# Kernel optimization log

Hardware: AMD Instinct MI355X
Metric: run time of the kernel (lower is better)

Reference implementation:

```python
import jax, jax.numpy as jnp
import numpy as np

EPS = 1e-5
NEG = -1000000000.0

def _layernorm(x, g, b):
    m = x.mean(-1, keepdims=True)
    v = ((x - m) ** 2).mean(-1, keepdims=True)
    return (x - m) / jnp.sqrt(v + EPS) * g + b

D_MODEL, N_HEADS, D_K, D_V, D_FF = 768, 12, 64, 64, 3072
VOCAB, MAX_POS, N_LAYERS = 32000, 2048, 2
B, S = 2, 2048

def setup_inputs() -> dict:
    key = jax.random.key(0)
    ks = jax.random.split(key, 16)
    sc = 0.02
    L = N_LAYERS
    return {
        "inputs": jax.random.randint(ks[0], (B, S), 0, VOCAB, dtype=jnp.int64) if jax.config.jax_enable_x64 else jax.random.randint(ks[0], (B, S), 0, VOCAB, dtype=jnp.int32),
        "attention_mask": jax.random.randint(ks[1], (B, S), 0, 2, dtype=jnp.int32),
        "emb": jax.random.normal(ks[2], (VOCAB, D_MODEL), jnp.float32) * sc,
        "pos_emb": jax.random.normal(ks[3], (MAX_POS, D_MODEL), jnp.float32) * sc,
        "wq": jax.random.normal(ks[4], (L, D_MODEL, N_HEADS * D_K), jnp.float32) * sc,
        "wk": jax.random.normal(ks[5], (L, D_MODEL, N_HEADS * D_K), jnp.float32) * sc,
        "wv": jax.random.normal(ks[6], (L, D_MODEL, N_HEADS * D_V), jnp.float32) * sc,
        "wo": jax.random.normal(ks[7], (L, N_HEADS * D_V, D_MODEL), jnp.float32) * sc,
        "ln1_g": jnp.ones((L, D_MODEL), jnp.float32),
        "ln1_b": jnp.zeros((L, D_MODEL), jnp.float32),
        "w1": jax.random.normal(ks[8], (L, D_MODEL, D_FF), jnp.float32) * sc,
        "b1": jnp.zeros((L, D_FF), jnp.float32),
        "w2": jax.random.normal(ks[9], (L, D_FF, D_MODEL), jnp.float32) * sc,
        "b2": jnp.zeros((L, D_MODEL), jnp.float32),
        "ln2_g": jnp.ones((L, D_MODEL), jnp.float32),
        "ln2_b": jnp.zeros((L, D_MODEL), jnp.float32),
    }

def reference(inputs, attention_mask, emb, pos_emb, wq, wk, wv, wo,
              ln1_g, ln1_b, w1, b1, w2, b2, ln2_g, ln2_b):
    b, s = inputs.shape
    x = emb[inputs] + pos_emb[jnp.arange(s)][None, :, :]  # [B,S,D]
    # combined mask: True where pad token OR strictly-upper (future) position
    sub = jnp.triu(jnp.ones((s, s), dtype=bool), k=1)            # [S,S]
    pad = (attention_mask == 0)[:, None, :]                      # [B,1,S]
    mask = (pad | sub[None, :, :])[:, None, :, :]                # [B,1,S,S] -> broadcast over heads
    # FAITHFUL to source: masked_fill(attention_mask == 0, -1e9) fills where mask is FALSE
    scale = 1.0 / float(np.sqrt(D_K))
    attns = []
    for l in range(N_LAYERS):
        q = (x @ wq[l]).reshape(b, s, N_HEADS, D_K).transpose(0, 2, 1, 3)  # [B,H,S,dk]
        k = (x @ wk[l]).reshape(b, s, N_HEADS, D_K).transpose(0, 2, 1, 3)
        v = (x @ wv[l]).reshape(b, s, N_HEADS, D_V).transpose(0, 2, 1, 3)
        scores = jnp.einsum('bhqd,bhkd->bhqk', q, k) * scale
        scores = jnp.where(mask, scores, NEG)  # fill -1e9 where mask == False (as in source)
        attn = jax.nn.softmax(scores, axis=-1)
        ctx = jnp.einsum('bhqk,bhkd->bhqd', attn, v)
        ctx = ctx.transpose(0, 2, 1, 3).reshape(b, s, N_HEADS * D_V)
        x = _layernorm(ctx @ wo[l] + x, ln1_g[l], ln1_b[l])
        ff = jnp.maximum(x @ w1[l] + b1[l], 0.0) @ w2[l] + b2[l]
        x = _layernorm(ff + x, ln2_g[l], ln2_b[l])
        attns.append(attn)
    return x, jnp.stack(attns)  # [B,S,D], [L,B,H,S,S]
```

## Files before the change

kernel.cpp:

```cpp
#include <hip/hip_runtime.h>
#include <math.h>

#define DM 768
#define NH 12
#define DK 64
#define DFF 3072
#define BB 2
#define SS 2048
#define NL 2

typedef __attribute__((ext_vector_type(8))) short short8;
typedef __attribute__((ext_vector_type(4))) float f32x4;

__device__ inline unsigned short f2bf(float f) {
    unsigned int u = __float_as_uint(f);
    u += 0x7fffu + ((u >> 16) & 1u);
    return (unsigned short)(u >> 16);
}
__device__ inline float bf2f(unsigned short h) {
    return __uint_as_float(((unsigned int)h) << 16);
}

#define GL16(g, l) __builtin_amdgcn_global_load_lds( \
    (const __attribute__((address_space(1))) void*)(g), \
    (__attribute__((address_space(3))) void*)(l), 16, 0, 0)

__global__ __launch_bounds__(256) void embed_kernel(
    const int* __restrict__ toks, const float* __restrict__ emb,
    const float* __restrict__ pos, float* __restrict__ x,
    unsigned short* __restrict__ xb)
{
    int rs = blockIdx.x;
    int s = rs & (SS - 1);
    int tok = toks[rs];
    int t = threadIdx.x;
    const float* e = emb + (size_t)tok * DM;
    const float* p = pos + (size_t)s * DM;
    float* xr = x + (size_t)rs * DM;
    unsigned short* xbr = xb + (size_t)rs * DM;
#pragma unroll
    for (int i = 0; i < 3; ++i) {
        int c = t + 256 * i;
        float v = e[c] + p[c];
        xr[c] = v;
        xbr[c] = f2bf(v);
    }
}

__global__ __launch_bounds__(256) void prep_weights(
    const float* __restrict__ wq, const float* __restrict__ wk,
    const float* __restrict__ wv, const float* __restrict__ wo,
    const float* __restrict__ w1, const float* __restrict__ w2,
    unsigned short* __restrict__ wt)
{
    __shared__ float tile[32][33];
    int id = blockIdx.x;
    int l = id / 6912; id -= l * 6912;
    unsigned short* wtl = wt + (size_t)l * 7077888;
    const float* src; unsigned short* dst; int Kd, Nd, nt, kt;
    if (id < 2304) {
        int m = id / 576, r = id % 576;
        src = ((m == 0) ? wq : (m == 1) ? wk : (m == 2) ? wv : wo) + (size_t)l * DM * DM;
        dst = wtl + (size_t)m * 589824;
        Kd = 768; Nd = 768; nt = r / 24; kt = r % 24;
    } else if (id < 4608) {
        int r = id - 2304;
        src = w1 + (size_t)l * DM * DFF; dst = wtl + 2359296; Kd = 768; Nd = 3072;
        nt = r / 24; kt = r % 24;
    } else {
        int r = id - 4608;
        src = w2 + (size_t)l * DFF * DM; dst = wtl + 4718592; Kd = 3072; Nd = 768;
        nt = r / 96; kt = r % 96;
    }
    int n0 = nt * 32, k0 = kt * 32;
    int c = threadIdx.x & 31, rr = threadIdx.x >> 5;
#pragma unroll
    for (int i = 0; i < 32; i += 8)
        tile[rr + i][c] = src[(size_t)(k0 + rr + i) * Nd + n0 + c];
    __syncthreads();
#pragma unroll
    for (int i = 0; i < 32; i += 8)
        dst[(size_t)(n0 + rr + i) * Kd + k0 + c] = f2bf(tile[c][rr + i]);
}

__global__ __launch_bounds__(256) void transpose_v(
    const unsigned short* __restrict__ vb, unsigned short* __restrict__ vt)
{
    __shared__ unsigned short tile[32][33];
    int c0 = blockIdx.x * 32;
    int r0 = blockIdx.y * 32;
    int c = threadIdx.x & 31, rr = threadIdx.x >> 5;
#pragma unroll
    for (int i = 0; i < 32; i += 8)
        tile[rr + i][c] = vb[(size_t)(r0 + rr + i) * DM + c0 + c];
    __syncthreads();
    int b = r0 >> 11;
    int s0 = r0 & 2047;
#pragma unroll
    for (int i = 0; i < 32; i += 8)
        vt[((size_t)b * DM + c0 + rr + i) * SS + s0 + c] = tile[c][rr + i];
}

template<int OUT_MODE>
__global__ __launch_bounds__(256) void gemm_bt(
    const unsigned short* __restrict__ A, const unsigned short* __restrict__ Bt,
    const float* __restrict__ bias, void* __restrict__ Cv,
    int K, int lda, int ldb, int ldc)
{
    __shared__ unsigned short As[128 * 64];
    __shared__ unsigned short Bs[128 * 64];
    const int t = threadIdx.x;
    const int row0 = blockIdx.y * 128;
    const int col0 = blockIdx.x * 128;
    const int z = (OUT_MODE == 0) ? blockIdx.z : 0;
    if (OUT_MODE == 0) { A += (size_t)z * K; Bt += (size_t)z * K; }
    const int lane = t & 63, wid = t >> 6;
    const int wr = wid >> 1, wc = wid & 1;
    const int half = lane >> 4, lr = lane & 15;
    f32x4 acc[4][4] = {};

    for (int k0 = 0; k0 < K; k0 += 64) {
#pragma unroll
        for (int r_ = 0; r_ < 4; ++r_) {
            int o_ = r_ * 4096 + t * 16;
            int row_ = o_ >> 7;
            int cp_ = (o_ >> 4) & 7;
            int gk_ = (cp_ ^ (row_ & 7)) << 3;
            GL16(A + (size_t)(row0 + row_) * lda + k0 + gk_, (char*)As + o_);
            GL16(Bt + (size_t)(col0 + row_) * ldb + k0 + gk_, (char*)Bs + o_);
        }
        __syncthreads();
#pragma unroll
        for (int kk = 0; kk < 2; ++kk) {
            short8 a_[4], b_[4];
#pragma unroll
            for (int m = 0; m < 4; ++m) {
                int row_ = wr * 64 + m * 16 + lr;
                a_[m] = *(const short8*)&As[row_ * 64 + (((kk * 4 + half) ^ (row_ & 7)) << 3)];
            }
#pragma unroll
            for (int n = 0; n < 4; ++n) {
                int row_ = wc * 64 + n * 16 + lr;
                b_[n] = *(const short8*)&Bs[row_ * 64 + (((kk * 4 + half) ^ (row_ & 7)) << 3)];
            }
#pragma unroll
            for (int m = 0; m < 4; ++m)
#pragma unroll
                for (int n = 0; n < 4; ++n)
                    acc[m][n] = __builtin_amdgcn_mfma_f32_16x16x32_bf16(a_[m], b_[n], acc[m][n], 0, 0, 0);
        }
        __syncthreads();
    }

#pragma unroll
    for (int m = 0; m < 4; ++m) {
#pragma unroll
        for (int n = 0; n < 4; ++n) {
            const int cidx = col0 + wc * 64 + n * 16 + lr;
            const float bv = bias ? bias[cidx] : 0.0f;
#pragma unroll
            for (int j = 0; j < 4; ++j) {
                const int r = row0 + wr * 64 + m * 16 + half * 4 + j;
                float v = acc[m][n][j] + bv;
                if (OUT_MODE == 2) v = fmaxf(v, 0.0f);
                if (OUT_MODE == 0) {
                    ((float*)Cv)[((size_t)z * 4096 + r) * ldc + cidx] = v;
                } else if (OUT_MODE == 4) {
                    int mi = (cidx >= 1536) ? 2 : (cidx >= 768 ? 1 : 0);
                    int cl = cidx - mi * 768;
                    ((unsigned short*)Cv)[((size_t)mi * 4096 + r) * 768 + cl] = f2bf(v);
                } else {
                    ((unsigned short*)Cv)[(size_t)r * ldc + cidx] = f2bf(v);
                }
            }
        }
    }
}

__global__ __launch_bounds__(256) void attn_fused(
    const unsigned short* __restrict__ qg, const unsigned short* __restrict__ kg,
    const unsigned short* __restrict__ vt, const int* __restrict__ amask,
    float* __restrict__ attnL, unsigned short* __restrict__ cb)
{
    __shared__ unsigned short Vs[2][64 * 128];
    __shared__ unsigned short Es[64 * 128];

    const int t = threadIdx.x;
    const int id = blockIdx.x;
    const int xcd = id & 7, idx = id >> 3;
    const int bh = xcd * 3 + (idx >> 5);
    const int qt = idx & 31;
    const int b = bh / NH, h = bh % NH;
    const int q0 = qt * 64;
    const int lane = t & 63, w = t >> 6;
    const int half = lane >> 4, lr = lane & 15;
    const int* am = amask + b * SS;

    const unsigned short* qbase = qg + ((size_t)b * SS + q0 + lr) * DM + h * DK + half * 8;
    short8 afq[4][2];
#pragma unroll
    for (int m = 0; m < 4; ++m) {
        afq[m][0] = *(const short8*)(qbase + m * 16 * DM);
        afq[m][1] = *(const short8*)(qbase + m * 16 * DM + 32);
    }

    const unsigned short* Kg = kg + (size_t)b * SS * DM + h * DK;
    const unsigned short* Vg = vt + ((size_t)b * DM + h * DK) * SS;

#define STAGE_V(kt, buf) { \
    _Pragma("unroll") \
    for (int r_ = 0; r_ < 4; ++r_) { \
        int o_ = r_ * 4096 + t * 16; \
        int d_ = o_ >> 8; \
        int cp_ = (o_ >> 4) & 15; \
        GL16(Vg + (size_t)d_ * SS + (kt) * 128 + ((cp_ ^ (d_ & 7)) << 3), (char*)Vs[buf] + o_); \
    } }

    float vsum[4][4] = {};
    for (int kt = 0; kt < 16; ++kt) {
#pragma unroll
        for (int nn = 0; nn < 2; ++nn) {
            const int kpos = kt * 128 + w * 32 + nn * 16 + lr;
            const unsigned short* kr = Kg + (size_t)kpos * DM;
            short8 bk0 = *(const short8*)(kr + half * 8);
            short8 bk1 = *(const short8*)(kr + 32 + half * 8);
            const bool pad = (am[kpos] == 0);
#pragma unroll
            for (int m = 0; m < 4; ++m) {
                f32x4 s = {};
                s = __builtin_amdgcn_mfma_f32_16x16x32_bf16(afq[m][0], bk0, s, 0, 0, 0);
                s = __builtin_amdgcn_mfma_f32_16x16x32_bf16(afq[m][1], bk1, s, 0, 0, 0);
#pragma unroll
                for (int j = 0; j < 4; ++j) {
                    int qpos = q0 + m * 16 + half * 4 + j;
                    if (pad || (kpos > qpos))
                        vsum[m][j] += __expf(0.125f * s[j]);
                }
            }
        }
    }
    STAGE_V(0, 0);
    __syncthreads();

    float* red = (float*)Es;
#pragma unroll
    for (int m = 0; m < 4; ++m)
#pragma unroll
        for (int j = 0; j < 4; ++j) {
            vsum[m][j] += __shfl_xor(vsum[m][j], 1, 64);
            vsum[m][j] += __shfl_xor(vsum[m][j], 2, 64);
            vsum[m][j] += __shfl_xor(vsum[m][j], 4, 64);
            vsum[m][j] += __shfl_xor(vsum[m][j], 8, 64);
        }
    if (lr == 0) {
#pragma unroll
        for (int m = 0; m < 4; ++m)
#pragma unroll
            for (int j = 0; j < 4; ++j)
                red[w * 64 + m * 16 + half * 4 + j] = vsum[m][j];
    }
    __syncthreads();
    if (t < 64) {
        float rs = red[t] + red[64 + t] + red[128 + t] + red[192 + t];
        red[256 + t] = (rs > 0.0f) ? 1.0f / rs : 0.0f;
    }
    __syncthreads();
    float rinv[4][4];
#pragma unroll
    for (int m = 0; m < 4; ++m)
#pragma unroll
        for (int j = 0; j < 4; ++j)
            rinv[m][j] = red[256 + m * 16 + half * 4 + j];
    __syncthreads();

    f32x4 ctxa[4] = {};
    float* ab = attnL + ((size_t)bh * SS + q0) * SS;
    for (int kt = 0; kt < 16; ++kt) {
        if (kt == 0) {
            asm volatile("s_waitcnt vmcnt(0)" ::: "memory");
        } else {
            asm volatile("s_waitcnt vmcnt(8)" ::: "memory");
        }
        __builtin_amdgcn_s_barrier();

        short8 bk[2][2];
        bool pad[2];
#pragma unroll
        for (int nn = 0; nn < 2; ++nn) {
            const int kpos = kt * 128 + w * 32 + nn * 16 + lr;
            const unsigned short* kr = Kg + (size_t)kpos * DM;
            bk[nn][0] = *(const short8*)(kr + half * 8);
            bk[nn][1] = *(const short8*)(kr + 32 + half * 8);
            pad[nn] = (am[kpos] == 0);
        }
        __builtin_amdgcn_sched_barrier(0);
        if (kt < 15) STAGE_V(kt + 1, (kt + 1) & 1);

#pragma unroll
        for (int nn = 0; nn < 2; ++nn) {
            const int krl = w * 32 + nn * 16 + lr;
            const int kpos = kt * 128 + krl;
#pragma unroll
            for (int m = 0; m < 4; ++m) {
                f32x4 s = {};
                s = __builtin_amdgcn_mfma_f32_16x16x32_bf16(afq[m][0], bk[nn][0], s, 0, 0, 0);
                s = __builtin_amdgcn_mfma_f32_16x16x32_bf16(afq[m][1], bk[nn][1], s, 0, 0, 0);
#pragma unroll
                for (int j = 0; j < 4; ++j) {
                    int row = m * 16 + half * 4 + j;
                    int qpos = q0 + row;
                    bool keep = pad[nn] || (kpos > qpos);
                    float e = keep ? __expf(0.125f * s[j]) * rinv[m][j] : 0.0f;
                    *((unsigned short*)((char*)Es + row * 256 + ((krl * 2) ^ ((row & 7) << 4)))) = f2bf(e);
                }
            }
        }
        asm volatile("s_waitcnt lgkmcnt(0)" ::: "memory");
        __builtin_amdgcn_s_barrier();

        const char* vbuf = (const char*)Vs[kt & 1];
#pragma unroll
        for (int ks = 0; ks < 4; ++ks) {
            const int dl = w * 16 + lr;
            const int cv = ks * 4 + half;
            short8 bv = *(const short8*)(vbuf + dl * 256 + ((cv ^ (dl & 7)) << 4));
#pragma unroll
            for (int m = 0; m < 4; ++m) {
                short8 ae = *(const short8*)((const char*)Es + (m * 16 + lr) * 256 +
                                             ((ks * 64 + half * 16) ^ ((lr & 7) << 4)));
                ctxa[m] = __builtin_amdgcn_mfma_f32_16x16x32_bf16(ae, bv, ctxa[m], 0, 0, 0);
            }
        }

        {
            const int prow = t >> 2, pg = t & 3;
            const char* erow = (const char*)Es + prow * 256;
            const int swz = (prow & 7) << 4;
            float* drow = ab + (size_t)prow * SS + kt * 128;
#pragma unroll
            for (int c = 0; c < 4; ++c) {
                const int chunk = pg * 4 + c;
                short8 ev = *(const short8*)(erow + ((chunk * 16) ^ swz));
                float* dst = drow + chunk * 8;
                f32x4 o0, o1;
                o0[0] = bf2f((unsigned short)ev[0]); o0[1] = bf2f((unsigned short)ev[1]);
                o0[2] = bf2f((unsigned short)ev[2]); o0[3] = bf2f((unsigned short)ev[3]);
                o1[0] = bf2f((unsigned short)ev[4]); o1[1] = bf2f((unsigned short)ev[5]);
                o1[2] = bf2f((unsigned short)ev[6]); o1[3] = bf2f((unsigned short)ev[7]);
                *(f32x4*)dst = o0;
                *(f32x4*)(dst + 4) = o1;
            }
        }
    }

#pragma unroll
    for (int m = 0; m < 4; ++m)
#pragma unroll
        for (int j = 0; j < 4; ++j) {
            int row = m * 16 + half * 4 + j;
            cb[((size_t)b * SS + q0 + row) * DM + h * DK + w * 16 + lr] = f2bf(ctxa[m][j]);
        }
#undef STAGE_V
}

__global__ __launch_bounds__(256) void add_ln_kernel(
    const float* __restrict__ p0, const float* __restrict__ p1,
    const float* __restrict__ bias, const float* __restrict__ xin,
    const float* __restrict__ g, const float* __restrict__ bta,
    float* __restrict__ xout, unsigned short* __restrict__ xbout)
{
    int row = blockIdx.x;
    int t = threadIdx.x;
    const float* a0 = p0 + (size_t)row * DM;
    const float* a1 = p1 + (size_t)row * DM;
    const float* xr = xin + (size_t)row * DM;
    float* orow = xout + (size_t)row * DM;
    unsigned short* obr = xbout + (size_t)row * DM;
    __shared__ float red[256];
    float v[3];
    float sum = 0.0f;
#pragma unroll
    for (int i = 0; i < 3; ++i) {
        int c = t + 256 * i;
        v[i] = a0[c] + a1[c] + xr[c] + (bias ? bias[c] : 0.0f);
        sum += v[i];
    }
    red[t] = sum;
    __syncthreads();
    for (int s = 128; s > 0; s >>= 1) {
        if (t < s) red[t] += red[t + s];
        __syncthreads();
    }
    float mean = red[0] * (1.0f / DM);
    __syncthreads();
    float sq = 0.0f;
#pragma unroll
    for (int i = 0; i < 3; ++i) {
        float d = v[i] - mean;
        sq += d * d;
    }
    red[t] = sq;
    __syncthreads();
    for (int s = 128; s > 0; s >>= 1) {
        if (t < s) red[t] += red[t + s];
        __syncthreads();
    }
    float inv = 1.0f / sqrtf(red[0] * (1.0f / DM) + 1e-5f);
#pragma unroll
    for (int i = 0; i < 3; ++i) {
        int c = t + 256 * i;
        float ov = (v[i] - mean) * inv * g[c] + bta[c];
        orow[c] = ov;
        obr[c] = f2bf(ov);
    }
}

extern "C" void kernel_launch(void* const* d_in, const int* in_sizes, int n_in,
                              void* d_out, int out_size, void* d_ws, size_t ws_size,
                              hipStream_t stream)
{
    const int*   toks  = (const int*)d_in[0];
    const int*   amask = (const int*)d_in[1];
    const float* emb   = (const float*)d_in[2];
    const float* pos   = (const float*)d_in[3];
    const float* wq    = (const float*)d_in[4];
    const float* wk    = (const float*)d_in[5];
    const float* wv    = (const float*)d_in[6];
    const float* wo    = (const float*)d_in[7];
    const float* ln1g  = (const float*)d_in[8];
    const float* ln1b  = (const float*)d_in[9];
    const float* w1    = (const float*)d_in[10];
    const float* b1    = (const float*)d_in[11];
    const float* w2    = (const float*)d_in[12];
    const float* b2    = (const float*)d_in[13];
    const float* ln2g  = (const float*)d_in[14];
    const float* ln2b  = (const float*)d_in[15];

    float* out = (float*)d_out;
    char*  wsb = (char*)d_ws;

    const size_t ROWS = (size_t)BB * SS;
    const size_t XSZ  = ROWS * DM;
    const size_t ATTN_L = (size_t)BB * NH * SS * SS;

    float*          x    = (float*)(wsb);
    unsigned short* xb   = (unsigned short*)(wsb + 12582912);
    unsigned short* qb   = (unsigned short*)(wsb + 18874368);
    unsigned short* kbuf = (unsigned short*)(wsb + 25165824);
    unsigned short* vb   = (unsigned short*)(wsb + 31457280);
    unsigned short* cb   = (unsigned short*)(wsb + 37748736);
    float*          p0   = (float*)(wsb + 44040192);
    unsigned short* vt   = (unsigned short*)(wsb + 69206016);
    unsigned short* ffb  = (unsigned short*)(wsb + 69206016);
    unsigned short* wt   = (unsigned short*)(wsb + 94371840);

    float* attn_out = out + XSZ;

    embed_kernel<<<ROWS, 256, 0, stream>>>(toks, emb, pos, x, xb);
    prep_weights<<<13824, 256, 0, stream>>>(wq, wk, wv, wo, w1, w2, wt);

    for (int l = 0; l < NL; ++l) {
        unsigned short* QKVT = wt + (size_t)l * 7077888;
        unsigned short* WOT  = QKVT + 1769472;
        unsigned short* W1T  = QKVT + 2359296;
        unsigned short* W2T  = QKVT + 4718592;

        gemm_bt<4><<<dim3(18, 32), 256, 0, stream>>>(xb, QKVT, nullptr, qb, DM, DM, DM, DM);
        transpose_v<<<dim3(24, 128), 256, 0, stream>>>(vb, vt);

        float* attnL = attn_out + (size_t)l * ATTN_L;
        attn_fused<<<768, 256, 0, stream>>>(qb, kbuf, vt, amask, attnL, cb);

        gemm_bt<0><<<dim3(6, 32, 2), 256, 0, stream>>>(cb, WOT, nullptr, p0, 384, DM, DM, DM);
        add_ln_kernel<<<ROWS, 256, 0, stream>>>(p0, p0 + XSZ, nullptr, x,
                                                ln1g + l * DM, ln1b + l * DM, x, xb);

        gemm_bt<2><<<dim3(24, 32), 256, 0, stream>>>(xb, W1T, b1 + (size_t)l * DFF, ffb, DM, DM, DM, DFF);
        gemm_bt<0><<<dim3(6, 32, 2), 256, 0, stream>>>(ffb, W2T, nullptr, p0, 1536, DFF, DFF, DM);

        float* xdst = (l == NL - 1) ? out : x;
        add_ln_kernel<<<ROWS, 256, 0, stream>>>(p0, p0 + XSZ, b2 + (size_t)l * DM, x,
                                                ln2g + l * DM, ln2b + l * DM, xdst, xb);
    }
}
```

Before: 740.4 us.

## Split fused attention into row-sum pass and PV pass kernels

The fused attention kernel is split in two. A separate kernel computes the softmax denominators with 32-row query tiles over 1536 blocks, giving more parallelism, and writes the reciprocals to workspace that aliases p0. The second kernel reads those reciprocals and does the normalized probability write and PV product. It drops V double buffering for single-buffer staging with an extra barrier per tile and raises wave priority around the MFMA section. This trades an extra launch and recomputed QK^T for better occupancy and lower LDS use, but loses the overlap of V loads with compute.

```diff
diff --git a/kernel.cpp b/kernel.cpp
--- a/kernel.cpp
+++ b/kernel.cpp
@@ -177,12 +177,84 @@
     }
 }
 
-__global__ __launch_bounds__(256) void attn_fused(
+__global__ __launch_bounds__(256) void attn_sums(
+    const unsigned short* __restrict__ qg, const unsigned short* __restrict__ kg,
+    const int* __restrict__ amask, float* __restrict__ rsum)
+{
+    __shared__ float red[128];
+    const int t = threadIdx.x;
+    const int id = blockIdx.x;
+    const int xcd = id & 7, idx = id >> 3;
+    const int bh = xcd * 3 + (idx >> 6);
+    const int qt = idx & 63;
+    const int b = bh / NH, h = bh % NH;
+    const int q0 = qt * 32;
+    const int lane = t & 63, w = t >> 6;
+    const int half = lane >> 4, lr = lane & 15;
+    const int* am = amask + b * SS;
+
+    const unsigned short* qbase = qg + ((size_t)b * SS + q0 + lr) * DM + h * DK + half * 8;
+    short8 afq[2][2];
+#pragma unroll
+    for (int m = 0; m < 2; ++m) {
+        afq[m][0] = *(const short8*)(qbase + m * 16 * DM);
+        afq[m][1] = *(const short8*)(qbase + m * 16 * DM + 32);
+    }
+    const unsigned short* Kg = kg + (size_t)b * SS * DM + h * DK;
+
+    float vsum[2][4] = {};
+    for (int kt = 0; kt < 16; ++kt) {
+#pragma unroll
+        for (int nn = 0; nn < 2; ++nn) {
+            const int kpos = kt * 128 + w * 32 + nn * 16 + lr;
+            const unsigned short* kr = Kg + (size_t)kpos * DM;
+            short8 bk0 = *(const short8*)(kr + half * 8);
+            short8 bk1 = *(const short8*)(kr + 32 + half * 8);
+            const bool pad = (am[kpos] == 0);
+#pragma unroll
+            for (int m = 0; m < 2; ++m) {
+                f32x4 s = {};
+                s = __builtin_amdgcn_mfma_f32_16x16x32_bf16(afq[m][0], bk0, s, 0, 0, 0);
+                s = __builtin_amdgcn_mfma_f32_16x16x32_bf16(afq[m][1], bk1, s, 0, 0, 0);
+#pragma unroll
+                for (int j = 0; j < 4; ++j) {
+                    int qpos = q0 + m * 16 + half * 4 + j;
+                    if (pad || (kpos > qpos))
+                        vsum[m][j] += __expf(0.125f * s[j]);
+                }
+            }
+        }
+    }
+#pragma unroll
+    for (int m = 0; m < 2; ++m)
+#pragma unroll
+        for (int j = 0; j < 4; ++j) {
+            vsum[m][j] += __shfl_xor(vsum[m][j], 1, 64);
+            vsum[m][j] += __shfl_xor(vsum[m][j], 2, 64);
+            vsum[m][j] += __shfl_xor(vsum[m][j], 4, 64);
+            vsum[m][j] += __shfl_xor(vsum[m][j], 8, 64);
+        }
+    if (lr == 0) {
+#pragma unroll
+        for (int m = 0; m < 2; ++m)
+#pragma unroll
+            for (int j = 0; j < 4; ++j)
+                red[w * 32 + m * 16 + half * 4 + j] = vsum[m][j];
+    }
+    __syncthreads();
+    if (t < 32) {
+        float rs = red[t] + red[32 + t] + red[64 + t] + red[96 + t];
+        rsum[(size_t)bh * SS + q0 + t] = (rs > 0.0f) ? 1.0f / rs : 0.0f;
+    }
+}
+
+__global__ __launch_bounds__(256) void attn_pv(
     const unsigned short* __restrict__ qg, const unsigned short* __restrict__ kg,
     const unsigned short* __restrict__ vt, const int* __restrict__ amask,
-    float* __restrict__ attnL, unsigned short* __restrict__ cb)
-{
-    __shared__ unsigned short Vs[2][64 * 128];
+    const float* __restrict__ rsumG, float* __restrict__ attnL,
+    unsigned short* __restrict__ cb)
+{
+    __shared__ unsigned short Vs[64 * 128];
     __shared__ unsigned short Es[64 * 128];
 
     const int t = threadIdx.x;
@@ -203,24 +275,34 @@
         afq[m][0] = *(const short8*)(qbase + m * 16 * DM);
         afq[m][1] = *(const short8*)(qbase + m * 16 * DM + 32);
     }
+    float rinv[4][4];
+#pragma unroll
+    for (int m = 0; m < 4; ++m)
+#pragma unroll
+        for (int j = 0; j < 4; ++j)
+            rinv[m][j] = rsumG[(size_t)bh * SS + q0 + m * 16 + half * 4 + j];
 
     const unsigned short* Kg = kg + (size_t)b * SS * DM + h * DK;
     const unsigned short* Vg = vt + ((size_t)b * DM + h * DK) * SS;
 
-#define STAGE_V(kt, buf) { \
+#define STAGE_V(kt) { \
     _Pragma("unroll") \
     for (int r_ = 0; r_ < 4; ++r_) { \
         int o_ = r_ * 4096 + t * 16; \
         int d_ = o_ >> 8; \
         int cp_ = (o_ >> 4) & 15; \
-        GL16(Vg + (size_t)d_ * SS + (kt) * 128 + ((cp_ ^ (d_ & 7)) << 3), (char*)Vs[buf] + o_); \
+        GL16(Vg + (size_t)d_ * SS + (kt) * 128 + ((cp_ ^ (d_ & 7)) << 3), (char*)Vs + o_); \
     } }
 
-    float vsum[4][4] = {};
+    f32x4 ctxa[4] = {};
+    float* ab = attnL + ((size_t)bh * SS + q0) * SS;
     for (int kt = 0; kt < 16; ++kt) {
+        STAGE_V(kt);
+
 #pragma unroll
         for (int nn = 0; nn < 2; ++nn) {
-            const int kpos = kt * 128 + w * 32 + nn * 16 + lr;
+            const int krl = w * 32 + nn * 16 + lr;
+            const int kpos = kt * 128 + krl;
             const unsigned short* kr = Kg + (size_t)kpos * DM;
             short8 bk0 = *(const short8*)(kr + half * 8);
             short8 bk1 = *(const short8*)(kr + 32 + half * 8);
@@ -232,98 +314,23 @@
                 s = __builtin_amdgcn_mfma_f32_16x16x32_bf16(afq[m][1], bk1, s, 0, 0, 0);
 #pragma unroll
                 for (int j = 0; j < 4; ++j) {
-                    int qpos = q0 + m * 16 + half * 4 + j;
-                    if (pad || (kpos > qpos))
-                        vsum[m][j] += __expf(0.125f * s[j]);
-                }
-            }
-        }
-    }
-    STAGE_V(0, 0);
-    __syncthreads();
-
-    float* red = (float*)Es;
-#pragma unroll
-    for (int m = 0; m < 4; ++m)
-#pragma unroll
-        for (int j = 0; j < 4; ++j) {
-            vsum[m][j] += __shfl_xor(vsum[m][j], 1, 64);
-            vsum[m][j] += __shfl_xor(vsum[m][j], 2, 64);
-            vsum[m][j] += __shfl_xor(vsum[m][j], 4, 64);
-            vsum[m][j] += __shfl_xor(vsum[m][j], 8, 64);
-        }
-    if (lr == 0) {
-#pragma unroll
-        for (int m = 0; m < 4; ++m)
-#pragma unroll
-            for (int j = 0; j < 4; ++j)
-                red[w * 64 + m * 16 + half * 4 + j] = vsum[m][j];
-    }
-    __syncthreads();
-    if (t < 64) {
-        float rs = red[t] + red[64 + t] + red[128 + t] + red[192 + t];
-        red[256 + t] = (rs > 0.0f) ? 1.0f / rs : 0.0f;
-    }
-    __syncthreads();
-    float rinv[4][4];
-#pragma unroll
-    for (int m = 0; m < 4; ++m)
-#pragma unroll
-        for (int j = 0; j < 4; ++j)
-            rinv[m][j] = red[256 + m * 16 + half * 4 + j];
-    __syncthreads();
-
-    f32x4 ctxa[4] = {};
-    float* ab = attnL + ((size_t)bh * SS + q0) * SS;
-    for (int kt = 0; kt < 16; ++kt) {
-        if (kt == 0) {
-            asm volatile("s_waitcnt vmcnt(0)" ::: "memory");
-        } else {
-            asm volatile("s_waitcnt vmcnt(8)" ::: "memory");
-        }
-        __builtin_amdgcn_s_barrier();
-
-        short8 bk[2][2];
-        bool pad[2];
-#pragma unroll
-        for (int nn = 0; nn < 2; ++nn) {
-            const int kpos = kt * 128 + w * 32 + nn * 16 + lr;
-            const unsigned short* kr = Kg + (size_t)kpos * DM;
-            bk[nn][0] = *(const short8*)(kr + half * 8);
-            bk[nn][1] = *(const short8*)(kr + 32 + half * 8);
-            pad[nn] = (am[kpos] == 0);
-        }
-        __builtin_amdgcn_sched_barrier(0);
-        if (kt < 15) STAGE_V(kt + 1, (kt + 1) & 1);
-
-#pragma unroll
-        for (int nn = 0; nn < 2; ++nn) {
-            const int krl = w * 32 + nn * 16 + lr;
-            const int kpos = kt * 128 + krl;
-#pragma unroll
-            for (int m = 0; m < 4; ++m) {
-                f32x4 s = {};
-                s = __builtin_amdgcn_mfma_f32_16x16x32_bf16(afq[m][0], bk[nn][0], s, 0, 0, 0);
-                s = __builtin_amdgcn_mfma_f32_16x16x32_bf16(afq[m][1], bk[nn][1], s, 0, 0, 0);
-#pragma unroll
-                for (int j = 0; j < 4; ++j) {
                     int row = m * 16 + half * 4 + j;
                     int qpos = q0 + row;
-                    bool keep = pad[nn] || (kpos > qpos);
+                    bool keep = pad || (kpos > qpos);
                     float e = keep ? __expf(0.125f * s[j]) * rinv[m][j] : 0.0f;
                     *((unsigned short*)((char*)Es + row * 256 + ((krl * 2) ^ ((row & 7) << 4)))) = f2bf(e);
                 }
             }
         }
-        asm volatile("s_waitcnt lgkmcnt(0)" ::: "memory");
+        asm volatile("s_waitcnt vmcnt(0) lgkmcnt(0)" ::: "memory");
         __builtin_amdgcn_s_barrier();
 
-        const char* vbuf = (const char*)Vs[kt & 1];
+        __builtin_amdgcn_s_setprio(1);
 #pragma unroll
         for (int ks = 0; ks < 4; ++ks) {
             const int dl = w * 16 + lr;
             const int cv = ks * 4 + half;
-            short8 bv = *(const short8*)(vbuf + dl * 256 + ((cv ^ (dl & 7)) << 4));
+            short8 bv = *(const short8*)((const char*)Vs + dl * 256 + ((cv ^ (dl & 7)) << 4));
 #pragma unroll
             for (int m = 0; m < 4; ++m) {
                 short8 ae = *(const short8*)((const char*)Es + (m * 16 + lr) * 256 +
@@ -331,6 +338,7 @@
                 ctxa[m] = __builtin_amdgcn_mfma_f32_16x16x32_bf16(ae, bv, ctxa[m], 0, 0, 0);
             }
         }
+        __builtin_amdgcn_s_setprio(0);
 
         {
             const int prow = t >> 2, pg = t & 3;
@@ -351,6 +359,7 @@
                 *(f32x4*)(dst + 4) = o1;
             }
         }
+        __builtin_amdgcn_s_barrier();
     }
 
 #pragma unroll
@@ -450,6 +459,7 @@
     unsigned short* vb   = (unsigned short*)(wsb + 31457280);
     unsigned short* cb   = (unsigned short*)(wsb + 37748736);
     float*          p0   = (float*)(wsb + 44040192);
+    float*          rsum = (float*)(wsb + 44040192);
     unsigned short* vt   = (unsigned short*)(wsb + 69206016);
     unsigned short* ffb  = (unsigned short*)(wsb + 69206016);
     unsigned short* wt   = (unsigned short*)(wsb + 94371840);
@@ -469,7 +479,8 @@
         transpose_v<<<dim3(24, 128), 256, 0, stream>>>(vb, vt);
 
         float* attnL = attn_out + (size_t)l * ATTN_L;
-        attn_fused<<<768, 256, 0, stream>>>(qb, kbuf, vt, amask, attnL, cb);
+        attn_sums<<<1536, 256, 0, stream>>>(qb, kbuf, amask, rsum);
+        attn_pv<<<768, 256, 0, stream>>>(qb, kbuf, vt, amask, rsum, attnL, cb);
 
         gemm_bt<0><<<dim3(6, 32, 2), 256, 0, stream>>>(cb, WOT, nullptr, p0, 384, DM, DM, DM);
         add_ln_kernel<<<ROWS, 256, 0, stream>>>(p0, p0 + XSZ, nullptr, x,
```

New measurement: 839.3 us. +13.4%, slower.
